# Kernel optimization log

Measured on AMD Instinct MI355X. Metric: run time of the kernel, lower is better.

## Reference

```python
import jax, jax.numpy as jnp
import numpy as np

N_NODES = 50000
N_EDGES = 500000
D = 128          # n_features
HID = 64         # explainer MLP hidden dim
TEMP = 5.0       # temp[0], epoch-0 temperature
SAMPLE_BIAS = 0.0


def setup_inputs() -> dict:
    key = jax.random.key(0)
    ks = jax.random.split(key, 8)
    embeds = jax.random.normal(ks[0], (N_NODES, D), dtype=jnp.float32)
    W1 = jax.random.normal(ks[1], (3 * D, HID), dtype=jnp.float32) * 0.05
    b1 = jnp.zeros((HID,), dtype=jnp.float32)
    W2 = jax.random.normal(ks[2], (HID, 1), dtype=jnp.float32) * 0.05
    b2 = jnp.zeros((1,), dtype=jnp.float32)
    u = jax.random.uniform(ks[3], (N_EDGES, 1), dtype=jnp.float32)
    src = jax.random.randint(ks[4], (N_EDGES,), 0, N_NODES, dtype=jnp.int64 if jax.config.jax_enable_x64 else jnp.int32)
    dst = jax.random.randint(ks[5], (N_EDGES,), 0, N_NODES, dtype=jnp.int64 if jax.config.jax_enable_x64 else jnp.int32)
    n = 0  # target node index within the subgraph
    return {"embeds": embeds, "W1": W1, "b1": b1, "W2": W2, "b2": b2,
            "u": u, "src": src, "dst": dst, "n": n}


def reference(embeds, W1, b1, W2, b2, u, src, dst, n):
    # --- _create_explainer_input: edge-wise gather + concat with target node embed ---
    row_embeds = embeds[src]                                   # [E, D]
    col_embeds = embeds[dst]                                   # [E, D]
    node_data = jnp.broadcast_to(embeds[n][None, :], row_embeds.shape)  # [E, D]
    inputs = jnp.concatenate([row_embeds, col_embeds, node_data], axis=1)  # [E, 3D]
    # --- explainer_model: Linear(3D,64) -> ReLU -> Linear(64,1) ---
    h = jax.nn.relu(inputs @ W1 + b1)                          # [E, HID]
    sampling_weights = h @ W2 + b2                             # [E, 1]
    # --- _sample_graph (training=True): Gumbel-sigmoid ---
    bias = SAMPLE_BIAS + 0.0001
    eps = (bias - (1.0 - bias)) * u + (1.0 - bias)             # U(bias, 1-bias)
    gate_inputs = jnp.log(eps) - jnp.log1p(-eps)
    mask = jax.nn.sigmoid((gate_inputs + sampling_weights) / TEMP)
    return mask.squeeze(-1)                                    # [E]
```

## Files before the change

### kernel.cpp

```cpp
#include <hip/hip_runtime.h>
#include <hip/hip_bf16.h>
#include <string.h>


#define D 128
#define HID 64

typedef __attribute__((ext_vector_type(8))) short short8;
typedef __attribute__((ext_vector_type(4))) float f32x4;
typedef _Float16 h2 __attribute__((ext_vector_type(2)));

union U32H2 { unsigned u; h2 h; };

__device__ inline unsigned short f2bf(float f) {
    union { float f; unsigned int u; } x;
    x.f = f;
    unsigned int r = x.u + 0x7FFFu + ((x.u >> 16) & 1u);
    return (unsigned short)(r >> 16);
}

__device__ inline unsigned int f2e5u(float f) {
    _Float16 h = (_Float16)f;
    unsigned short u;
    __builtin_memcpy(&u, &h, 2);
    unsigned short r = (unsigned short)(u + 0x7Fu + ((u >> 8) & 1u));
    return (unsigned int)(r >> 8) & 0xFFu;
}

__device__ inline unsigned packh(float lo, float hi) {
    _Float16 l = (_Float16)lo, h = (_Float16)hi;
    unsigned short ul, uh;
    __builtin_memcpy(&ul, &l, 2);
    __builtin_memcpy(&uh, &h, 2);
    return (unsigned)ul | ((unsigned)uh << 16);
}

__device__ inline h2 relu2(h2 x) {
#if __has_builtin(__builtin_elementwise_max)
    return __builtin_elementwise_max(x, (h2)((_Float16)0));
#else
    h2 r;
    r[0] = x[0] > (_Float16)0 ? x[0] : (_Float16)0;
    r[1] = x[1] > (_Float16)0 ? x[1] : (_Float16)0;
    return r;
#endif
}

__device__ inline float dot2acc(h2 a, h2 b, float c) {
#if __has_builtin(__builtin_amdgcn_fdot2)
    return __builtin_amdgcn_fdot2(a, b, c, false);
#else
    c = fmaf((float)a[0], (float)b[0], c);
    return fmaf((float)a[1], (float)b[1], c);
#endif
}

__global__ __launch_bounds__(256) void pg_prep(
    const float* __restrict__ embeds, const float* __restrict__ W1,
    const float* __restrict__ b1, const float* __restrict__ W2,
    const int* __restrict__ nidx,
    unsigned short* __restrict__ bfrag,
    unsigned* __restrict__ cnodeh, unsigned* __restrict__ w2h)
{
    int t = threadIdx.x;
    if (blockIdx.x < 64) {
        int i    = blockIdx.x * 256 + t;
        int j    = i & 7;
        int lane = (i >> 3) & 63;
        int ct   = (i >> 9) & 7;
        int ks   = i >> 12;
        int k    = ks * 32 + (lane >> 4) * 8 + j;
        int col  = ct * 16 + (lane & 15);
        float w  = (col < HID) ? W1[k * HID + col]
                               : W1[(D + k) * HID + (col - HID)];
        bfrag[i] = f2bf(w);
    } else {
        __shared__ float cs[HID];
        if (t < HID) {
            int n = nidx[0];
            const float* nr = embeds + (size_t)n * D;
            float c = b1[t];
            #pragma unroll 8
            for (int k = 0; k < D; ++k)
                c = fmaf(nr[k], W1[(2 * D + k) * HID + t], c);
            cs[t] = c;
        }
        __syncthreads();
        if (t < 32) {
            int wi = t >> 1, sub = t & 1;
            int j = 4 * wi + sub;
            cnodeh[t] = packh(cs[j], cs[j + 2]);
            w2h[t]    = packh(W2[j], W2[j + 2]);
        }
    }
}

__global__ __launch_bounds__(256) void pg_nodes(
    const float* __restrict__ embeds, const unsigned short* __restrict__ bfrag,
    unsigned char* __restrict__ P, int N, int NTILES)
{
    __shared__ unsigned char st[4][16 * 144];

    int wave  = threadIdx.x >> 6;
    int lane  = threadIdx.x & 63;
    int ntile = blockIdx.x * 4 + wave;
    if (ntile >= NTILES) return;

    int kg = lane >> 4;
    int nr = ntile * 16 + (lane & 15);
    if (nr >= N) nr = N - 1;
    const float* row = embeds + (size_t)nr * D + kg * 8;

    short8 af[4];
    #pragma unroll
    for (int ks = 0; ks < 4; ++ks) {
        float4 v0 = *reinterpret_cast<const float4*>(row + ks * 32);
        float4 v1 = *reinterpret_cast<const float4*>(row + ks * 32 + 4);
        union { float f; unsigned u; } c[8];
        c[0].f = v0.x; c[1].f = v0.y; c[2].f = v0.z; c[3].f = v0.w;
        c[4].f = v1.x; c[5].f = v1.y; c[6].f = v1.z; c[7].f = v1.w;
        union { unsigned u[4]; short8 s; } pk;
        #pragma unroll
        for (int p = 0; p < 4; ++p)
            pk.u[p] = (c[2 * p + 1].u & 0xFFFF0000u) | (c[2 * p].u >> 16);
        af[ks] = pk.s;
    }

    const short8* gw = reinterpret_cast<const short8*>(bfrag);

    f32x4 acc[8];
    #pragma unroll
    for (int ct = 0; ct < 8; ++ct) acc[ct] = (f32x4){0.f, 0.f, 0.f, 0.f};

    #pragma unroll
    for (int ct = 0; ct < 8; ++ct) {
        #pragma unroll
        for (int ks = 0; ks < 4; ++ks) {
            short8 wf = gw[(ks * 8 + ct) * 64 + lane];
            acc[ct] = __builtin_amdgcn_mfma_f32_16x16x32_bf16(wf, af[ks], acc[ct], 0, 0, 0);
        }
    }

    #pragma unroll
    for (int ct = 0; ct < 8; ++ct) {
        unsigned w = f2e5u(acc[ct][0])
                   | (f2e5u(acc[ct][1]) << 8)
                   | (f2e5u(acc[ct][2]) << 16)
                   | (f2e5u(acc[ct][3]) << 24);
        *reinterpret_cast<unsigned*>(&st[wave][(lane & 15) * 144 + ct * 16 + kg * 4]) = w;
    }
    #pragma unroll
    for (int h = 0; h < 2; ++h) {
        int c   = lane + h * 64;
        int r   = c >> 3;
        int off = (c & 7) * 16;
        uint4 v = *reinterpret_cast<const uint4*>(&st[wave][r * 144 + off]);
        int node = ntile * 16 + r;
        if (node < N)
            *reinterpret_cast<uint4*>(P + (size_t)node * 128 + off) = v;
    }
}

__device__ inline float mlp16(uint4 A, uint4 B,
                              const unsigned* cnv, const unsigned* w2v)
{
    float sw = 0.f;
    unsigned aw[4] = {A.x, A.y, A.z, A.w};
    unsigned bw[4] = {B.x, B.y, B.z, B.w};
    #pragma unroll
    for (int w = 0; w < 4; ++w) {
        U32H2 a0, a1, b0, b1, c0, c1, W0, W1v;
        a0.u = (aw[w] << 8) & 0xFF00FF00u;
        a1.u =  aw[w]       & 0xFF00FF00u;
        b0.u = (bw[w] << 8) & 0xFF00FF00u;
        b1.u =  bw[w]       & 0xFF00FF00u;
        c0.u = cnv[2 * w];  c1.u = cnv[2 * w + 1];
        W0.u = w2v[2 * w];  W1v.u = w2v[2 * w + 1];
        h2 h0 = relu2(a0.h + b0.h + c0.h);
        h2 h1 = relu2(a1.h + b1.h + c1.h);
        sw = dot2acc(h0, W0.h, sw);
        sw = dot2acc(h1, W1v.h, sw);
    }
    return sw;
}

__device__ inline float gumbel_sigmoid(float uu, float sw) {
    float a = 0.9999f - 0.9998f * uu;
    float b = 0.0001f + 0.9998f * uu;
    float gate = __logf(__fdividef(a, b));
    float x = (gate + sw) * 0.2f;
    return __fdividef(1.f, 1.f + __expf(-x));
}

__global__ __launch_bounds__(256) void pg_edge(
    const unsigned char* __restrict__ P,
    const unsigned* __restrict__ cnodeh, const unsigned* __restrict__ w2h,
    const float* __restrict__ b2, const float* __restrict__ u,
    const int* __restrict__ src, const int* __restrict__ dst,
    float* __restrict__ out, int E)
{
    int r    = threadIdx.x & 3;
    int quad = (blockIdx.x * 256 + threadIdx.x) >> 2;
    int e0   = quad * 2;
    if (e0 >= E) return;
    bool two = (e0 + 1 < E);

    unsigned cnv[8], w2v[8];
    #pragma unroll
    for (int w = 0; w < 4; ++w) {
        int wi = 4 * r + w;
        cnv[2 * w]     = cnodeh[2 * wi];
        cnv[2 * w + 1] = cnodeh[2 * wi + 1];
        w2v[2 * w]     = w2h[2 * wi];
        w2v[2 * w + 1] = w2h[2 * wi + 1];
    }

    int2 sv, dv;
    if (two) {
        sv = *reinterpret_cast<const int2*>(src + e0);
        dv = *reinterpret_cast<const int2*>(dst + e0);
    } else {
        sv.x = sv.y = src[e0];
        dv.x = dv.y = dst[e0];
    }

    uint4 A0 = *reinterpret_cast<const uint4*>(P + (size_t)sv.x * 128 + r * 16);
    uint4 B0 = *reinterpret_cast<const uint4*>(P + (size_t)dv.x * 128 + 64 + r * 16);
    uint4 A1 = *reinterpret_cast<const uint4*>(P + (size_t)sv.y * 128 + r * 16);
    uint4 B1 = *reinterpret_cast<const uint4*>(P + (size_t)dv.y * 128 + 64 + r * 16);

    float sw0 = mlp16(A0, B0, cnv, w2v);
    float sw1 = mlp16(A1, B1, cnv, w2v);

    sw0 += __shfl_xor(sw0, 1); sw0 += __shfl_xor(sw0, 2);
    sw1 += __shfl_xor(sw1, 1); sw1 += __shfl_xor(sw1, 2);

    if (r == 0) {
        float bb = b2[0];
        if (two) {
            float2 uv = *reinterpret_cast<const float2*>(u + e0);
            float2 o;
            o.x = gumbel_sigmoid(uv.x, sw0 + bb);
            o.y = gumbel_sigmoid(uv.y, sw1 + bb);
            *reinterpret_cast<float2*>(out + e0) = o;
        } else {
            out[e0] = gumbel_sigmoid(u[e0], sw0 + bb);
        }
    }
}

extern "C" void kernel_launch(void* const* d_in, const int* in_sizes, int n_in,
                              void* d_out, int out_size, void* d_ws, size_t ws_size,
                              hipStream_t stream) {
    const float* embeds = (const float*)d_in[0];
    const float* W1     = (const float*)d_in[1];
    const float* b1     = (const float*)d_in[2];
    const float* W2     = (const float*)d_in[3];
    const float* b2     = (const float*)d_in[4];
    const float* u      = (const float*)d_in[5];
    const int*   src    = (const int*)d_in[6];
    const int*   dst    = (const int*)d_in[7];
    const int*   nidx   = (const int*)d_in[8];

    int E = in_sizes[6];
    int N = in_sizes[0] / D;
    int NTILES = (N + 15) / 16;

    unsigned short* bfrag = (unsigned short*)d_ws;
    unsigned* cnodeh = (unsigned*)(bfrag + 16384);
    unsigned* w2h    = cnodeh + 32;
    unsigned char* P = (unsigned char*)(w2h + 32);

    pg_prep<<<65, 256, 0, stream>>>(embeds, W1, b1, W2, nidx, bfrag, cnodeh, w2h);
    pg_nodes<<<(NTILES + 3) / 4, 256, 0, stream>>>(embeds, bfrag, P, N, NTILES);

    long threads = ((long)E + 1) / 2 * 4;
    int blocks = (int)((threads + 255) / 256);
    pg_edge<<<blocks, 256, 0, stream>>>(P, cnodeh, w2h, b2, u,
                                        src, dst, (float*)d_out, E);
}
```

Before: 36.67 us.

## Process four edges per quad, vectorize constant loads, pack fp8 conversion

The edge kernel now handles four edges per 4-lane group instead of two, using int4/float4 loads for indices, u and outputs and issuing eight gathers per thread for more memory-level parallelism. The node-constant and W2 half vectors are re-laid out per lane group so each thread loads them with four uint4 reads instead of sixteen scalar loads. The node kernel's float-to-e5m2 conversion now uses packed RTZ half conversion plus a byte permute in place of per-element conversion. Tradeoffs are higher register pressure, half the number of threads in the edge kernel, and slightly different rounding from the RTZ half conversion.

```diff
diff --git a/kernel.cpp b/kernel.cpp
--- a/kernel.cpp
+++ b/kernel.cpp
@@ -17,14 +17,6 @@
     x.f = f;
     unsigned int r = x.u + 0x7FFFu + ((x.u >> 16) & 1u);
     return (unsigned short)(r >> 16);
-}
-
-__device__ inline unsigned int f2e5u(float f) {
-    _Float16 h = (_Float16)f;
-    unsigned short u;
-    __builtin_memcpy(&u, &h, 2);
-    unsigned short r = (unsigned short)(u + 0x7Fu + ((u >> 8) & 1u));
-    return (unsigned int)(r >> 8) & 0xFFu;
 }
 
 __device__ inline unsigned packh(float lo, float hi) {
@@ -55,12 +47,18 @@
 #endif
 }
 
+__device__ inline unsigned pkrtz_u32(float a, float b) {
+    auto v = __builtin_amdgcn_cvt_pkrtz(a, b);
+    unsigned u;
+    __builtin_memcpy(&u, &v, 4);
+    return u;
+}
+
 __global__ __launch_bounds__(256) void pg_prep(
     const float* __restrict__ embeds, const float* __restrict__ W1,
     const float* __restrict__ b1, const float* __restrict__ W2,
     const int* __restrict__ nidx,
-    unsigned short* __restrict__ bfrag,
-    unsigned* __restrict__ cnodeh, unsigned* __restrict__ w2h)
+    unsigned short* __restrict__ bfrag, unsigned* __restrict__ cnw)
 {
     int t = threadIdx.x;
     if (blockIdx.x < 64) {
@@ -89,8 +87,9 @@
         if (t < 32) {
             int wi = t >> 1, sub = t & 1;
             int j = 4 * wi + sub;
-            cnodeh[t] = packh(cs[j], cs[j + 2]);
-            w2h[t]    = packh(W2[j], W2[j + 2]);
+            int r = t >> 3, q = t & 7;
+            cnw[r * 16 + q]     = packh(cs[j], cs[j + 2]);
+            cnw[r * 16 + 8 + q] = packh(W2[j], W2[j + 2]);
         }
     }
 }
@@ -143,10 +142,11 @@
 
     #pragma unroll
     for (int ct = 0; ct < 8; ++ct) {
-        unsigned w = f2e5u(acc[ct][0])
-                   | (f2e5u(acc[ct][1]) << 8)
-                   | (f2e5u(acc[ct][2]) << 16)
-                   | (f2e5u(acc[ct][3]) << 24);
+        unsigned p0 = pkrtz_u32(acc[ct][0], acc[ct][1]);
+        unsigned p1 = pkrtz_u32(acc[ct][2], acc[ct][3]);
+        unsigned u0 = p0 + 0x007F007Fu + ((p0 >> 8) & 0x00010001u);
+        unsigned u1 = p1 + 0x007F007Fu + ((p1 >> 8) & 0x00010001u);
+        unsigned w = __builtin_amdgcn_perm(u1, u0, 0x07050301u);
         *reinterpret_cast<unsigned*>(&st[wave][(lane & 15) * 144 + ct * 16 + kg * 4]) = w;
     }
     #pragma unroll
@@ -162,7 +162,7 @@
 }
 
 __device__ inline float mlp16(uint4 A, uint4 B,
-                              const unsigned* cnv, const unsigned* w2v)
+                              const unsigned* cn, const unsigned* w2)
 {
     float sw = 0.f;
     unsigned aw[4] = {A.x, A.y, A.z, A.w};
@@ -174,8 +174,8 @@
         a1.u =  aw[w]       & 0xFF00FF00u;
         b0.u = (bw[w] << 8) & 0xFF00FF00u;
         b1.u =  bw[w]       & 0xFF00FF00u;
-        c0.u = cnv[2 * w];  c1.u = cnv[2 * w + 1];
-        W0.u = w2v[2 * w];  W1v.u = w2v[2 * w + 1];
+        c0.u = cn[2 * w];  c1.u = cn[2 * w + 1];
+        W0.u = w2[2 * w];  W1v.u = w2[2 * w + 1];
         h2 h0 = relu2(a0.h + b0.h + c0.h);
         h2 h1 = relu2(a1.h + b1.h + c1.h);
         sw = dot2acc(h0, W0.h, sw);
@@ -193,58 +193,67 @@
 }
 
 __global__ __launch_bounds__(256) void pg_edge(
-    const unsigned char* __restrict__ P,
-    const unsigned* __restrict__ cnodeh, const unsigned* __restrict__ w2h,
+    const unsigned char* __restrict__ P, const uint4* __restrict__ cnw4,
     const float* __restrict__ b2, const float* __restrict__ u,
     const int* __restrict__ src, const int* __restrict__ dst,
     float* __restrict__ out, int E)
 {
     int r    = threadIdx.x & 3;
     int quad = (blockIdx.x * 256 + threadIdx.x) >> 2;
-    int e0   = quad * 2;
+    int e0   = quad * 4;
     if (e0 >= E) return;
-    bool two = (e0 + 1 < E);
-
-    unsigned cnv[8], w2v[8];
-    #pragma unroll
-    for (int w = 0; w < 4; ++w) {
-        int wi = 4 * r + w;
-        cnv[2 * w]     = cnodeh[2 * wi];
-        cnv[2 * w + 1] = cnodeh[2 * wi + 1];
-        w2v[2 * w]     = w2h[2 * wi];
-        w2v[2 * w + 1] = w2h[2 * wi + 1];
-    }
-
-    int2 sv, dv;
-    if (two) {
-        sv = *reinterpret_cast<const int2*>(src + e0);
-        dv = *reinterpret_cast<const int2*>(dst + e0);
+    bool full = (e0 + 4 <= E);
+
+    uint4 c0 = cnw4[r * 4 + 0], c1 = cnw4[r * 4 + 1];
+    uint4 c2 = cnw4[r * 4 + 2], c3 = cnw4[r * 4 + 3];
+    unsigned cn[8] = {c0.x, c0.y, c0.z, c0.w, c1.x, c1.y, c1.z, c1.w};
+    unsigned w2[8] = {c2.x, c2.y, c2.z, c2.w, c3.x, c3.y, c3.z, c3.w};
+
+    int si[4], di[4];
+    if (full) {
+        int4 sv = *reinterpret_cast<const int4*>(src + e0);
+        int4 dv = *reinterpret_cast<const int4*>(dst + e0);
+        si[0] = sv.x; si[1] = sv.y; si[2] = sv.z; si[3] = sv.w;
+        di[0] = dv.x; di[1] = dv.y; di[2] = dv.z; di[3] = dv.w;
     } else {
-        sv.x = sv.y = src[e0];
-        dv.x = dv.y = dst[e0];
-    }
-
-    uint4 A0 = *reinterpret_cast<const uint4*>(P + (size_t)sv.x * 128 + r * 16);
-    uint4 B0 = *reinterpret_cast<const uint4*>(P + (size_t)dv.x * 128 + 64 + r * 16);
-    uint4 A1 = *reinterpret_cast<const uint4*>(P + (size_t)sv.y * 128 + r * 16);
-    uint4 B1 = *reinterpret_cast<const uint4*>(P + (size_t)dv.y * 128 + 64 + r * 16);
-
-    float sw0 = mlp16(A0, B0, cnv, w2v);
-    float sw1 = mlp16(A1, B1, cnv, w2v);
-
-    sw0 += __shfl_xor(sw0, 1); sw0 += __shfl_xor(sw0, 2);
-    sw1 += __shfl_xor(sw1, 1); sw1 += __shfl_xor(sw1, 2);
+        int last = E - 1;
+        #pragma unroll
+        for (int i = 0; i < 4; ++i) {
+            int e = e0 + i <= last ? e0 + i : last;
+            si[i] = src[e]; di[i] = dst[e];
+        }
+    }
+
+    uint4 A[4], B[4];
+    #pragma unroll
+    for (int i = 0; i < 4; ++i) {
+        A[i] = *reinterpret_cast<const uint4*>(P + (size_t)si[i] * 128 + r * 16);
+        B[i] = *reinterpret_cast<const uint4*>(P + (size_t)di[i] * 128 + 64 + r * 16);
+    }
+
+    float sw[4];
+    #pragma unroll
+    for (int i = 0; i < 4; ++i) {
+        float s = mlp16(A[i], B[i], cn, w2);
+        s += __shfl_xor(s, 1);
+        s += __shfl_xor(s, 2);
+        sw[i] = s;
+    }
 
     if (r == 0) {
         float bb = b2[0];
-        if (two) {
-            float2 uv = *reinterpret_cast<const float2*>(u + e0);
-            float2 o;
-            o.x = gumbel_sigmoid(uv.x, sw0 + bb);
-            o.y = gumbel_sigmoid(uv.y, sw1 + bb);
-            *reinterpret_cast<float2*>(out + e0) = o;
+        if (full) {
+            float4 uv = *reinterpret_cast<const float4*>(u + e0);
+            float4 o;
+            o.x = gumbel_sigmoid(uv.x, sw[0] + bb);
+            o.y = gumbel_sigmoid(uv.y, sw[1] + bb);
+            o.z = gumbel_sigmoid(uv.z, sw[2] + bb);
+            o.w = gumbel_sigmoid(uv.w, sw[3] + bb);
+            *reinterpret_cast<float4*>(out + e0) = o;
         } else {
-            out[e0] = gumbel_sigmoid(u[e0], sw0 + bb);
+            #pragma unroll
+            for (int i = 0; i < 4; ++i)
+                if (e0 + i < E) out[e0 + i] = gumbel_sigmoid(u[e0 + i], sw[i] + bb);
         }
     }
 }
@@ -267,15 +276,14 @@
     int NTILES = (N + 15) / 16;
 
     unsigned short* bfrag = (unsigned short*)d_ws;
-    unsigned* cnodeh = (unsigned*)(bfrag + 16384);
-    unsigned* w2h    = cnodeh + 32;
-    unsigned char* P = (unsigned char*)(w2h + 32);
-
-    pg_prep<<<65, 256, 0, stream>>>(embeds, W1, b1, W2, nidx, bfrag, cnodeh, w2h);
+    unsigned* cnw = (unsigned*)(bfrag + 16384);
+    unsigned char* P = (unsigned char*)(cnw + 64);
+
+    pg_prep<<<65, 256, 0, stream>>>(embeds, W1, b1, W2, nidx, bfrag, cnw);
     pg_nodes<<<(NTILES + 3) / 4, 256, 0, stream>>>(embeds, bfrag, P, N, NTILES);
 
-    long threads = ((long)E + 1) / 2 * 4;
-    int blocks = (int)((threads + 255) / 256);
-    pg_edge<<<blocks, 256, 0, stream>>>(P, cnodeh, w2h, b2, u,
+    long quads = ((long)E + 3) / 4;
+    int blocks = (int)((quads * 4 + 255) / 256);
+    pg_edge<<<blocks, 256, 0, stream>>>(P, (const uint4*)cnw, b2, u,
                                         src, dst, (float*)d_out, E);
 }
```

New measurement: 36.98 us. Within noise of the previous version (+0.9%).

## Fuse weight-fragment prep into node projection kernel and pack edge constants

Applied to the files above, without the earlier changes.

Removes the separate prep launch. Each node block now builds the bf16 W1 MFMA fragments in its own 32KB of LDS, and the last block computes the target-node constant and W2 halves. The fp8 conversion is rewritten to use packed RTZ half conversion plus a byte permute. Node constants and W2 are stored interleaved, so edge threads fetch them with four uint4 loads. The cost is that every one of ~780 node blocks re-reads and converts all of W1, which adds L2 traffic and a syncthreads, and the large LDS use may reduce occupancy. RTZ conversion also changes rounding slightly.

```diff
diff --git a/kernel.cpp b/kernel.cpp
--- a/kernel.cpp
+++ b/kernel.cpp
@@ -17,14 +17,6 @@
     x.f = f;
     unsigned int r = x.u + 0x7FFFu + ((x.u >> 16) & 1u);
     return (unsigned short)(r >> 16);
-}
-
-__device__ inline unsigned int f2e5u(float f) {
-    _Float16 h = (_Float16)f;
-    unsigned short u;
-    __builtin_memcpy(&u, &h, 2);
-    unsigned short r = (unsigned short)(u + 0x7Fu + ((u >> 8) & 1u));
-    return (unsigned int)(r >> 8) & 0xFFu;
 }
 
 __device__ inline unsigned packh(float lo, float hi) {
@@ -55,26 +47,22 @@
 #endif
 }
 
-__global__ __launch_bounds__(256) void pg_prep(
+__device__ inline unsigned pkrtz_u32(float a, float b) {
+    auto v = __builtin_amdgcn_cvt_pkrtz(a, b);
+    unsigned u;
+    __builtin_memcpy(&u, &v, 4);
+    return u;
+}
+
+__global__ __launch_bounds__(256) void pg_nodes_fused(
     const float* __restrict__ embeds, const float* __restrict__ W1,
     const float* __restrict__ b1, const float* __restrict__ W2,
-    const int* __restrict__ nidx,
-    unsigned short* __restrict__ bfrag,
-    unsigned* __restrict__ cnodeh, unsigned* __restrict__ w2h)
+    const int* __restrict__ nidx, unsigned* __restrict__ cnw,
+    unsigned char* __restrict__ P, int N, int NTILES)
 {
     int t = threadIdx.x;
-    if (blockIdx.x < 64) {
-        int i    = blockIdx.x * 256 + t;
-        int j    = i & 7;
-        int lane = (i >> 3) & 63;
-        int ct   = (i >> 9) & 7;
-        int ks   = i >> 12;
-        int k    = ks * 32 + (lane >> 4) * 8 + j;
-        int col  = ct * 16 + (lane & 15);
-        float w  = (col < HID) ? W1[k * HID + col]
-                               : W1[(D + k) * HID + (col - HID)];
-        bfrag[i] = f2bf(w);
-    } else {
+
+    if (blockIdx.x == gridDim.x - 1) {
         __shared__ float cs[HID];
         if (t < HID) {
             int n = nidx[0];
@@ -89,20 +77,33 @@
         if (t < 32) {
             int wi = t >> 1, sub = t & 1;
             int j = 4 * wi + sub;
-            cnodeh[t] = packh(cs[j], cs[j + 2]);
-            w2h[t]    = packh(W2[j], W2[j + 2]);
-        }
-    }
-}
-
-__global__ __launch_bounds__(256) void pg_nodes(
-    const float* __restrict__ embeds, const unsigned short* __restrict__ bfrag,
-    unsigned char* __restrict__ P, int N, int NTILES)
-{
+            int r = t >> 3, q = t & 7;
+            cnw[r * 16 + q]     = packh(cs[j], cs[j + 2]);
+            cnw[r * 16 + 8 + q] = packh(W2[j], W2[j + 2]);
+        }
+        return;
+    }
+
+    __shared__ unsigned short wl[16384];
     __shared__ unsigned char st[4][16 * 144];
 
-    int wave  = threadIdx.x >> 6;
-    int lane  = threadIdx.x & 63;
+    #pragma unroll 4
+    for (int it = 0; it < 64; ++it) {
+        int i    = it * 256 + t;
+        int j    = i & 7;
+        int lane = (i >> 3) & 63;
+        int ct   = (i >> 9) & 7;
+        int ks   = i >> 12;
+        int k    = ks * 32 + (lane >> 4) * 8 + j;
+        int col  = ct * 16 + (lane & 15);
+        float w  = (col < HID) ? W1[k * HID + col]
+                               : W1[(D + k) * HID + (col - HID)];
+        wl[i] = f2bf(w);
+    }
+    __syncthreads();
+
+    int wave  = t >> 6;
+    int lane  = t & 63;
     int ntile = blockIdx.x * 4 + wave;
     if (ntile >= NTILES) return;
 
@@ -126,7 +127,7 @@
         af[ks] = pk.s;
     }
 
-    const short8* gw = reinterpret_cast<const short8*>(bfrag);
+    const short8* wl8 = reinterpret_cast<const short8*>(wl);
 
     f32x4 acc[8];
     #pragma unroll
@@ -136,17 +137,18 @@
     for (int ct = 0; ct < 8; ++ct) {
         #pragma unroll
         for (int ks = 0; ks < 4; ++ks) {
-            short8 wf = gw[(ks * 8 + ct) * 64 + lane];
+            short8 wf = wl8[(ks * 8 + ct) * 64 + lane];
             acc[ct] = __builtin_amdgcn_mfma_f32_16x16x32_bf16(wf, af[ks], acc[ct], 0, 0, 0);
         }
     }
 
     #pragma unroll
     for (int ct = 0; ct < 8; ++ct) {
-        unsigned w = f2e5u(acc[ct][0])
-                   | (f2e5u(acc[ct][1]) << 8)
-                   | (f2e5u(acc[ct][2]) << 16)
-                   | (f2e5u(acc[ct][3]) << 24);
+        unsigned p0 = pkrtz_u32(acc[ct][0], acc[ct][1]);
+        unsigned p1 = pkrtz_u32(acc[ct][2], acc[ct][3]);
+        unsigned u0 = p0 + 0x007F007Fu + ((p0 >> 8) & 0x00010001u);
+        unsigned u1 = p1 + 0x007F007Fu + ((p1 >> 8) & 0x00010001u);
+        unsigned w = __builtin_amdgcn_perm(u1, u0, 0x07050301u);
         *reinterpret_cast<unsigned*>(&st[wave][(lane & 15) * 144 + ct * 16 + kg * 4]) = w;
     }
     #pragma unroll
@@ -162,7 +164,7 @@
 }
 
 __device__ inline float mlp16(uint4 A, uint4 B,
-                              const unsigned* cnv, const unsigned* w2v)
+                              const unsigned* cn, const unsigned* w2)
 {
     float sw = 0.f;
     unsigned aw[4] = {A.x, A.y, A.z, A.w};
@@ -174,8 +176,8 @@
         a1.u =  aw[w]       & 0xFF00FF00u;
         b0.u = (bw[w] << 8) & 0xFF00FF00u;
         b1.u =  bw[w]       & 0xFF00FF00u;
-        c0.u = cnv[2 * w];  c1.u = cnv[2 * w + 1];
-        W0.u = w2v[2 * w];  W1v.u = w2v[2 * w + 1];
+        c0.u = cn[2 * w];  c1.u = cn[2 * w + 1];
+        W0.u = w2[2 * w];  W1v.u = w2[2 * w + 1];
         h2 h0 = relu2(a0.h + b0.h + c0.h);
         h2 h1 = relu2(a1.h + b1.h + c1.h);
         sw = dot2acc(h0, W0.h, sw);
@@ -193,8 +195,7 @@
 }
 
 __global__ __launch_bounds__(256) void pg_edge(
-    const unsigned char* __restrict__ P,
-    const unsigned* __restrict__ cnodeh, const unsigned* __restrict__ w2h,
+    const unsigned char* __restrict__ P, const uint4* __restrict__ cnw4,
     const float* __restrict__ b2, const float* __restrict__ u,
     const int* __restrict__ src, const int* __restrict__ dst,
     float* __restrict__ out, int E)
@@ -205,15 +206,10 @@
     if (e0 >= E) return;
     bool two = (e0 + 1 < E);
 
-    unsigned cnv[8], w2v[8];
-    #pragma unroll
-    for (int w = 0; w < 4; ++w) {
-        int wi = 4 * r + w;
-        cnv[2 * w]     = cnodeh[2 * wi];
-        cnv[2 * w + 1] = cnodeh[2 * wi + 1];
-        w2v[2 * w]     = w2h[2 * wi];
-        w2v[2 * w + 1] = w2h[2 * wi + 1];
-    }
+    uint4 c0 = cnw4[r * 4 + 0], c1 = cnw4[r * 4 + 1];
+    uint4 c2 = cnw4[r * 4 + 2], c3 = cnw4[r * 4 + 3];
+    unsigned cn[8] = {c0.x, c0.y, c0.z, c0.w, c1.x, c1.y, c1.z, c1.w};
+    unsigned w2[8] = {c2.x, c2.y, c2.z, c2.w, c3.x, c3.y, c3.z, c3.w};
 
     int2 sv, dv;
     if (two) {
@@ -229,8 +225,8 @@
     uint4 A1 = *reinterpret_cast<const uint4*>(P + (size_t)sv.y * 128 + r * 16);
     uint4 B1 = *reinterpret_cast<const uint4*>(P + (size_t)dv.y * 128 + 64 + r * 16);
 
-    float sw0 = mlp16(A0, B0, cnv, w2v);
-    float sw1 = mlp16(A1, B1, cnv, w2v);
+    float sw0 = mlp16(A0, B0, cn, w2);
+    float sw1 = mlp16(A1, B1, cn, w2);
 
     sw0 += __shfl_xor(sw0, 1); sw0 += __shfl_xor(sw0, 2);
     sw1 += __shfl_xor(sw1, 1); sw1 += __shfl_xor(sw1, 2);
@@ -266,16 +262,15 @@
     int N = in_sizes[0] / D;
     int NTILES = (N + 15) / 16;
 
-    unsigned short* bfrag = (unsigned short*)d_ws;
-    unsigned* cnodeh = (unsigned*)(bfrag + 16384);
-    unsigned* w2h    = cnodeh + 32;
-    unsigned char* P = (unsigned char*)(w2h + 32);
-
-    pg_prep<<<65, 256, 0, stream>>>(embeds, W1, b1, W2, nidx, bfrag, cnodeh, w2h);
-    pg_nodes<<<(NTILES + 3) / 4, 256, 0, stream>>>(embeds, bfrag, P, N, NTILES);
-
-    long threads = ((long)E + 1) / 2 * 4;
-    int blocks = (int)((threads + 255) / 256);
-    pg_edge<<<blocks, 256, 0, stream>>>(P, cnodeh, w2h, b2, u,
+    unsigned* cnw = (unsigned*)d_ws;
+    unsigned char* P = (unsigned char*)(cnw + 64);
+
+    int nb = (NTILES + 3) / 4 + 1;
+    pg_nodes_fused<<<nb, 256, 0, stream>>>(embeds, W1, b1, W2, nidx, cnw, P,
+                                           N, NTILES);
+
+    long quads = ((long)E + 1) / 2;
+    int blocks = (int)((quads * 4 + 255) / 256);
+    pg_edge<<<blocks, 256, 0, stream>>>(P, (const uint4*)cnw, b2, u,
                                         src, dst, (float*)d_out, E);
 }
```

After: 42.55 us. +16.1%, slower.
